# Kernel tuning notes

Measured on AMD Instinct MI355X. Metric: run time of the kernel, lower is better.

## Reference

```python
import jax, jax.numpy as jnp
import numpy as np


def setup_inputs() -> dict:
    key = jax.random.key(0)
    k1, k2, k3, k4 = jax.random.split(key, 4)
    d_in, d_out, B, T = 1024, 1024, 4, 2048
    scale = 1.0 / np.sqrt(d_in)
    return {
        "x": jax.random.normal(k1, (B, T, d_in), dtype=jnp.float32),
        "Wq": jax.random.normal(k2, (d_in, d_out), dtype=jnp.float32) * scale,
        "Wk": jax.random.normal(k3, (d_in, d_out), dtype=jnp.float32) * scale,
        "Wv": jax.random.normal(k4, (d_in, d_out), dtype=jnp.float32) * scale,
    }


def reference(x, Wq, Wk, Wv):
    # x: [B, T, d_in]; Wq/Wk/Wv: [d_in, d_out] (Linear, bias=False)
    q = jnp.einsum("btd,de->bte", x, Wq)
    k = jnp.einsum("btd,de->bte", x, Wk)
    v = jnp.einsum("btd,de->bte", x, Wv)
    d_out = k.shape[-1]
    scores = jnp.einsum("bqe,bke->bqk", q, k)  # [B, T, T]
    T = x.shape[1]
    causal = jnp.triu(jnp.ones((T, T), dtype=bool), k=1)  # True above diagonal
    scores = jnp.where(causal[None, :, :], -jnp.inf, scores)
    # original divides after masking; -inf stays -inf so math is identical
    att = jax.nn.softmax(scores / jnp.sqrt(jnp.asarray(d_out, scores.dtype)), axis=-1)
    # dropout p=0.0 -> identity
    return jnp.einsum("bqk,bke->bqe", att, v)
```

## Files before the change

kernel.cpp:

```cpp
#include <hip/hip_runtime.h>
#include <stdint.h>
#include <math.h>

typedef unsigned short u16;
typedef __bf16 bf16x8 __attribute__((ext_vector_type(8)));
typedef float f32x4 __attribute__((ext_vector_type(4)));

enum { M_QKV = 0, M_SCORE = 1, M_PV = 2 };

__device__ __forceinline__ u16 f2bf(float f) {
    union { float f; unsigned int u; } a; a.f = f;
    unsigned int u = a.u;
    u += 0x7FFFu + ((u >> 16) & 1u);
    return (u16)(u >> 16);
}

__device__ __forceinline__ void async_load16(const void* g, void* l) {
    __builtin_amdgcn_global_load_lds(
        (const __attribute__((address_space(1))) void*)g,
        (__attribute__((address_space(3))) void*)l,
        16, 0, 0);
}

template<int MODE, int TBM>
__device__ __forceinline__ void gemm_core(
    const u16* __restrict__ A, const u16* __restrict__ Bt,
    void* __restrict__ Cv, float* __restrict__ rowsum,
    int bm, int bn, int bz, int M, int N, int K, float kfac,
    u16* As, u16* Bs)
{
    constexpr int KB  = 64;
    constexpr int NI  = TBM / 32;
    constexpr int ACH = TBM / 32;
    constexpr int BCH = 4;

    const int tid  = threadIdx.x;
    const int lane = tid & 63;
    const int wv   = tid >> 6;
    const int wm   = wv >> 1;
    const int wn   = wv & 1;

    f32x4 acc[NI][4] = {};

    const int rowA0 = bm * TBM, rowB0 = bn * 128;
    const int lrow  = lane >> 3;
    const int lslot = lane & 7;
    const int sg    = (lslot ^ lrow) * 8;

    int kEnd = K;
    if (MODE == M_PV) { int ke = (bm + 1) * TBM; kEnd = ke < K ? ke : K; }

    const int lm   = lane & 15;
    const int quad = lane >> 4;
    const int rx   = lm & 7;

    for (int k0 = 0; k0 < kEnd; k0 += KB) {
        #pragma unroll
        for (int c = 0; c < ACH; ++c) {
            const int cc  = wv * ACH + c;
            const int row = cc * 8 + lrow;
            const u16* src;
            if (MODE == M_PV)
                src = &A[(size_t)(k0 >> 7) * 16384 + (size_t)row * 128 + (k0 & 127) + sg];
            else
                src = &A[(size_t)(rowA0 + row) * K + k0 + sg];
            async_load16(src, &As[cc * 512 + lane * 8]);
        }
        #pragma unroll
        for (int c = 0; c < BCH; ++c) {
            const int cc  = wv * BCH + c;
            const int row = cc * 8 + lrow;
            async_load16(&Bt[(size_t)(rowB0 + row) * K + k0 + sg], &Bs[cc * 512 + lane * 8]);
        }
        __syncthreads();

        #pragma unroll
        for (int h = 0; h < 2; ++h) {
            const int sl = (((h * 4 + quad) ^ rx) * 8);
            bf16x8 af[NI], bfr[4];
            #pragma unroll
            for (int i = 0; i < NI; ++i)
                af[i] = *reinterpret_cast<const bf16x8*>(
                    &As[(wm * (TBM / 2) + i * 16 + lm) * KB + sl]);
            #pragma unroll
            for (int j = 0; j < 4; ++j)
                bfr[j] = *reinterpret_cast<const bf16x8*>(
                    &Bs[(wn * 64 + j * 16 + lm) * KB + sl]);
            #pragma unroll
            for (int i = 0; i < NI; ++i)
                #pragma unroll
                for (int j = 0; j < 4; ++j)
                    acc[i][j] = __builtin_amdgcn_mfma_f32_16x16x32_bf16(af[i], bfr[j], acc[i][j], 0, 0, 0);
        }
        __syncthreads();
    }

    if (MODE == M_SCORE) {
        u16* E = (u16*)Cv;
        float rs[NI][4];
        #pragma unroll
        for (int i = 0; i < NI; ++i)
            #pragma unroll
            for (int g = 0; g < 4; ++g) rs[i][g] = 0.f;
        #pragma unroll
        for (int i = 0; i < NI; ++i)
            #pragma unroll
            for (int j = 0; j < 4; ++j) {
                const int rl = wm * (TBM / 2) + i * 16 + quad * 4;
                const int cl = wn * 64 + j * 16 + lm;
                const int c  = rowB0 + cl;
                #pragma unroll
                for (int g = 0; g < 4; ++g) {
                    const int r = rowA0 + rl + g;
                    float e = (c <= r) ? exp2f(acc[i][j][g] * kfac) : 0.f;
                    E[(size_t)(rl + g) * 128 + cl] = f2bf(e);
                    rs[i][g] += e;
                }
            }
        #pragma unroll
        for (int i = 0; i < NI; ++i)
            #pragma unroll
            for (int g = 0; g < 4; ++g) {
                float v = rs[i][g];
                v += __shfl_xor(v, 1); v += __shfl_xor(v, 2);
                v += __shfl_xor(v, 4); v += __shfl_xor(v, 8);
                rs[i][g] = v;
            }
        if (lm == 0) {
            #pragma unroll
            for (int i = 0; i < NI; ++i)
                #pragma unroll
                for (int g = 0; g < 4; ++g) {
                    const int r = rowA0 + wm * (TBM / 2) + i * 16 + quad * 4 + g;
                    atomicAdd(&rowsum[(size_t)bz * M + r], rs[i][g]);
                }
        }
    } else {
        float* C = (float*)Cv + (size_t)bz * ((size_t)M * N);
        #pragma unroll
        for (int i = 0; i < NI; ++i) {
            const int r0 = rowA0 + wm * (TBM / 2) + i * 16 + quad * 4;
            float inv[4];
            #pragma unroll
            for (int g = 0; g < 4; ++g)
                inv[g] = 1.f / rowsum[(size_t)bz * M + r0 + g];
            #pragma unroll
            for (int j = 0; j < 4; ++j) {
                const int c0 = rowB0 + wn * 64 + j * 16 + lm;
                #pragma unroll
                for (int g = 0; g < 4; ++g)
                    C[(size_t)(r0 + g) * N + c0] = acc[i][j][g] * inv[g];
            }
        }
    }
}

__global__ __launch_bounds__(512, 2)
void k_qkv2(const u16* __restrict__ Xb, const u16* __restrict__ Wt,
            u16* __restrict__ Q, int M, int N, int K)
{
    extern __shared__ __attribute__((aligned(16))) u16 S[];
    const int tid  = threadIdx.x;
    const int lane = tid & 63;
    const int wv   = tid >> 6;
    const int wm   = wv >> 2;
    const int wn   = wv & 3;
    const int bn   = blockIdx.x;
    const int bm   = blockIdx.y;
    const int rowA0 = bm * 128, rowB0 = bn * 256;

    const int lrow  = lane >> 3;
    const int lslot = lane & 7;
    const int sg    = (lslot ^ lrow) * 8;
    const int lm    = lane & 15;
    const int quad  = lane >> 4;
    const int rx    = lm & 7;

    f32x4 acc[4][4] = {};

    const int nt = K >> 6;

    auto stage = [&](int t, int b) {
        u16* As = S + b * 24576;
        u16* Bs = As + 8192;
        const int k0 = t << 6;
        #pragma unroll
        for (int c = 0; c < 2; ++c) {
            const int cc  = wv * 2 + c;
            const int row = cc * 8 + lrow;
            async_load16(&Xb[(size_t)(rowA0 + row) * K + k0 + sg], &As[cc * 512 + lane * 8]);
        }
        #pragma unroll
        for (int c = 0; c < 4; ++c) {
            const int cc  = wv * 4 + c;
            const int row = cc * 8 + lrow;
            async_load16(&Wt[(size_t)(rowB0 + row) * K + k0 + sg], &Bs[cc * 512 + lane * 8]);
        }
    };

    auto compute = [&](int b) {
        const u16* As = S + b * 24576;
        const u16* Bs = As + 8192;
        #pragma unroll
        for (int h = 0; h < 2; ++h) {
            const int sl = (((h * 4 + quad) ^ rx) * 8);
            bf16x8 af[4], bfr[4];
            #pragma unroll
            for (int i = 0; i < 4; ++i)
                af[i] = *reinterpret_cast<const bf16x8*>(
                    &As[(wm * 64 + i * 16 + lm) * 64 + sl]);
            #pragma unroll
            for (int j = 0; j < 4; ++j)
                bfr[j] = *reinterpret_cast<const bf16x8*>(
                    &Bs[(wn * 64 + j * 16 + lm) * 64 + sl]);
            #pragma unroll
            for (int i = 0; i < 4; ++i)
                #pragma unroll
                for (int j = 0; j < 4; ++j)
                    acc[i][j] = __builtin_amdgcn_mfma_f32_16x16x32_bf16(af[i], bfr[j], acc[i][j], 0, 0, 0);
        }
    };

    stage(0, 0);
    stage(1, 1);
    asm volatile("s_waitcnt vmcnt(6)" ::: "memory");
    __builtin_amdgcn_s_barrier();

    int cb = 0;
    #pragma unroll 1
    for (int t = 0; t < nt - 2; ++t) {
        int sb = cb + 2; if (sb >= 3) sb -= 3;
        stage(t + 2, sb);
        compute(cb);
        asm volatile("s_waitcnt vmcnt(6)" ::: "memory");
        __builtin_amdgcn_s_barrier();
        if (++cb == 3) cb = 0;
    }
    compute(cb);
    asm volatile("s_waitcnt vmcnt(0)" ::: "memory");
    __builtin_amdgcn_s_barrier();
    if (++cb == 3) cb = 0;
    compute(cb);

    u16* C = Q + (size_t)(bn >> 2) * ((size_t)M * 1024);
    const int cbase = (rowB0 & 1023) + wn * 64;
    #pragma unroll
    for (int i = 0; i < 4; ++i)
        #pragma unroll
        for (int j = 0; j < 4; ++j) {
            const int r0 = rowA0 + wm * 64 + i * 16 + quad * 4;
            const int c0 = cbase + j * 16 + lm;
            #pragma unroll
            for (int g = 0; g < 4; ++g)
                C[(size_t)(r0 + g) * 1024 + c0] = f2bf(acc[i][j][g]);
        }
}

__global__ __launch_bounds__(256)
void k_score_vt(const u16* __restrict__ Q, const u16* __restrict__ Kb,
                u16* __restrict__ Epk, float* __restrict__ rowsum,
                const u16* __restrict__ Vb, u16* __restrict__ Vt,
                int T, int D, float kfac, int nTri)
{
    __shared__ __attribute__((aligned(16))) u16 As[128 * 64];
    __shared__ __attribute__((aligned(16))) u16 Bs[128 * 64];
    __shared__ u16 tt[32][33];
    const int bz = blockIdx.z;

    if ((int)blockIdx.x < nTri) {
        const int idx = blockIdx.x;
        int bm = (int)((sqrtf(8.f * (float)idx + 1.f) - 1.f) * 0.5f);
        while (bm * (bm + 1) / 2 > idx) --bm;
        while ((bm + 1) * (bm + 2) / 2 <= idx) ++bm;
        const int bn = idx - bm * (bm + 1) / 2;
        u16* Etile = Epk + ((size_t)bz * nTri + idx) * 16384;
        gemm_core<M_SCORE, 128>(Q + (size_t)bz * T * D, Kb + (size_t)bz * T * D,
                                Etile, rowsum, bm, bn, bz, T, T, D, kfac, As, Bs);
    } else {
        const int t  = blockIdx.x - nTri;
        const int cx = t & 31;
        const int cy = t >> 5;
        const u16* V = Vb + (size_t)bz * T * D;
        u16*      Vo = Vt + (size_t)bz * D * T;
        const int c0 = cx * 32, r0 = cy * 32;
        const int tx = threadIdx.x & 31, ty = threadIdx.x >> 5;
        #pragma unroll
        for (int s = 0; s < 32; s += 8)
            tt[ty + s][tx] = V[(size_t)(r0 + ty + s) * D + c0 + tx];
        __syncthreads();
        #pragma unroll
        for (int s = 0; s < 32; s += 8)
            Vo[(size_t)(c0 + ty + s) * T + r0 + tx] = tt[tx][ty + s];
    }
}

__global__ __launch_bounds__(256)
void k_pv(const u16* __restrict__ Epk, const u16* __restrict__ Vt,
          float* __restrict__ out, const float* __restrict__ rowsum,
          int T, int D, int nTri)
{
    __shared__ __attribute__((aligned(16))) u16 As[128 * 64];
    __shared__ __attribute__((aligned(16))) u16 Bs[128 * 64];
    const int bz = blockIdx.z;
    const int bm = (gridDim.y - 1) - blockIdx.y;
    const u16* Arow = Epk + ((size_t)bz * nTri + (size_t)bm * (bm + 1) / 2) * 16384;
    gemm_core<M_PV, 128>(Arow, Vt + (size_t)bz * D * T,
                         out, (float*)rowsum, bm, blockIdx.x, bz,
                         T, D, T, 0.f, As, Bs);
}

__global__ __launch_bounds__(256)
void k_prep(const float* __restrict__ x,
            const float* __restrict__ W0, const float* __restrict__ W1,
            const float* __restrict__ W2,
            u16* __restrict__ Xb, u16* __restrict__ Wt, float* __restrict__ RS,
            int D, int nCX, int nW)
{
    const int bx = blockIdx.x;
    if (bx < nCX) {
        long long i = ((long long)bx * 256 + threadIdx.x) * 8;
        const float4 a = *(const float4*)(x + i);
        const float4 b = *(const float4*)(x + i + 4);
        union { u16 u[8]; float4 v; } r;
        r.u[0] = f2bf(a.x); r.u[1] = f2bf(a.y); r.u[2] = f2bf(a.z); r.u[3] = f2bf(a.w);
        r.u[4] = f2bf(b.x); r.u[5] = f2bf(b.y); r.u[6] = f2bf(b.z); r.u[7] = f2bf(b.w);
        *(float4*)(Xb + i) = r.v;
    } else if (bx < nCX + nW) {
        __shared__ u16 t[32][33];
        const int w  = bx - nCX;
        const int z  = w >> 10;
        const int rm = w & 1023;
        const float* W = z == 0 ? W0 : (z == 1 ? W1 : W2);
        u16* dst = Wt + (size_t)z * D * D;
        const int c0 = (rm & 31) * 32, r0 = (rm >> 5) * 32;
        const int tx = threadIdx.x & 31, ty = threadIdx.x >> 5;
        #pragma unroll
        for (int s = 0; s < 32; s += 8)
            t[ty + s][tx] = f2bf(W[(size_t)(r0 + ty + s) * D + c0 + tx]);
        __syncthreads();
        #pragma unroll
        for (int s = 0; s < 32; s += 8)
            dst[(size_t)(c0 + ty + s) * D + r0 + tx] = t[tx][ty + s];
    } else {
        const int t = bx - nCX - nW;
        ((float4*)RS)[t * 256 + threadIdx.x] = float4{0.f, 0.f, 0.f, 0.f};
    }
}

extern "C" void kernel_launch(void* const* d_in, const int* in_sizes, int n_in,
                              void* d_out, int out_size, void* d_ws, size_t ws_size,
                              hipStream_t stream)
{
    const int B = 4, T = 2048, D = 1024;
    const float* x  = (const float*)d_in[0];
    const float* Wq = (const float*)d_in[1];
    const float* Wk = (const float*)d_in[2];
    const float* Wv = (const float*)d_in[3];
    float* out = (float*)d_out;

    const size_t nX = (size_t)B * T * D;
    u16* Xb  = (u16*)d_ws;
    u16* Wt  = Xb + nX;
    u16* Epk = (u16*)d_ws;
    u16* Q   = Wt + 3 * (size_t)D * D;
    u16* Kb  = Q + nX;
    u16* Vb  = Kb + nX;
    u16* Vt  = Vb + nX;
    float* RS = (float*)(Vt + nX);

    const float kfac = 1.4426950408889634f / 32.0f;
    const int nTri128 = 136;
    const int nCX = (int)(nX / (8 * 256));
    const int nW  = 3 * (D / 32) * (D / 32);
    const int nRS = (B * T) / (4 * 256);

    static bool attr_done = false;
    if (!attr_done) {
        (void)hipFuncSetAttribute((const void*)k_qkv2,
                                  hipFuncAttributeMaxDynamicSharedMemorySize,
                                  147456);
        attr_done = true;
    }

    k_prep<<<dim3(nCX + nW + nRS), 256, 0, stream>>>(
        x, Wq, Wk, Wv, Xb, Wt, RS, D, nCX, nW);
    k_qkv2<<<dim3(3 * D / 256, (B * T) / 128), 512, 147456, stream>>>(
        Xb, Wt, Q, B * T, 3 * D, D);
    k_score_vt<<<dim3(nTri128 + (D / 32) * (T / 32), 1, B), 256, 0, stream>>>(
        Q, Kb, Epk, RS, Vb, Vt, T, D, kfac, nTri128);
    k_pv<<<dim3(D / 128, T / 128, B), 256, 0, stream>>>(
        Epk, Vt, out, RS, T, D, nTri128);
}
```

Measured before the change: 245.5 us.

## Double-buffer LDS tiles in score and PV GEMMs to overlap loads with MFMA

Replaces the single-buffered gemm_core with gemm2, which uses two LDS stages: it issues the async global-to-LDS loads for the next K tile before running the MFMAs on the current one, then waits on vmcnt and a barrier. This targets the load latency that sat exposed between the two __syncthreads per iteration. It doubles LDS use per block to 64 KB, which may reduce how many blocks fit on a CU, and it hardcodes the 128-row tile size.

```diff
diff --git a/kernel.cpp b/kernel.cpp
--- a/kernel.cpp
+++ b/kernel.cpp
@@ -6,7 +6,7 @@
 typedef __bf16 bf16x8 __attribute__((ext_vector_type(8)));
 typedef float f32x4 __attribute__((ext_vector_type(4)));
 
-enum { M_QKV = 0, M_SCORE = 1, M_PV = 2 };
+enum { M_SCORE = 1, M_PV = 2 };
 
 __device__ __forceinline__ u16 f2bf(float f) {
     union { float f; unsigned int u; } a; a.f = f;
@@ -22,91 +22,103 @@
         16, 0, 0);
 }
 
-template<int MODE, int TBM>
-__device__ __forceinline__ void gemm_core(
+template<int MODE>
+__device__ __forceinline__ void gemm2(
     const u16* __restrict__ A, const u16* __restrict__ Bt,
     void* __restrict__ Cv, float* __restrict__ rowsum,
     int bm, int bn, int bz, int M, int N, int K, float kfac,
     u16* As, u16* Bs)
 {
-    constexpr int KB  = 64;
-    constexpr int NI  = TBM / 32;
-    constexpr int ACH = TBM / 32;
-    constexpr int BCH = 4;
-
+    constexpr int KB = 64;
     const int tid  = threadIdx.x;
     const int lane = tid & 63;
     const int wv   = tid >> 6;
     const int wm   = wv >> 1;
     const int wn   = wv & 1;
 
-    f32x4 acc[NI][4] = {};
-
-    const int rowA0 = bm * TBM, rowB0 = bn * 128;
+    f32x4 acc[4][4] = {};
+
+    const int rowA0 = bm * 128, rowB0 = bn * 128;
     const int lrow  = lane >> 3;
     const int lslot = lane & 7;
     const int sg    = (lslot ^ lrow) * 8;
 
     int kEnd = K;
-    if (MODE == M_PV) { int ke = (bm + 1) * TBM; kEnd = ke < K ? ke : K; }
+    if (MODE == M_PV) { int ke = (bm + 1) * 128; kEnd = ke < K ? ke : K; }
+    const int nt = kEnd >> 6;
 
     const int lm   = lane & 15;
     const int quad = lane >> 4;
     const int rx   = lm & 7;
 
-    for (int k0 = 0; k0 < kEnd; k0 += KB) {
-        #pragma unroll
-        for (int c = 0; c < ACH; ++c) {
-            const int cc  = wv * ACH + c;
+    auto stage = [&](int t, int b) {
+        const int k0 = t << 6;
+        u16* as = As + b * 8192;
+        u16* bs = Bs + b * 8192;
+        #pragma unroll
+        for (int c = 0; c < 4; ++c) {
+            const int cc  = wv * 4 + c;
             const int row = cc * 8 + lrow;
-            const u16* src;
+            const u16* srcA;
             if (MODE == M_PV)
-                src = &A[(size_t)(k0 >> 7) * 16384 + (size_t)row * 128 + (k0 & 127) + sg];
+                srcA = &A[(size_t)(k0 >> 7) * 16384 + (size_t)row * 128 + (k0 & 127) + sg];
             else
-                src = &A[(size_t)(rowA0 + row) * K + k0 + sg];
-            async_load16(src, &As[cc * 512 + lane * 8]);
-        }
-        #pragma unroll
-        for (int c = 0; c < BCH; ++c) {
-            const int cc  = wv * BCH + c;
-            const int row = cc * 8 + lrow;
-            async_load16(&Bt[(size_t)(rowB0 + row) * K + k0 + sg], &Bs[cc * 512 + lane * 8]);
-        }
-        __syncthreads();
-
+                srcA = &A[(size_t)(rowA0 + row) * K + k0 + sg];
+            async_load16(srcA, &as[cc * 512 + lane * 8]);
+            async_load16(&Bt[(size_t)(rowB0 + row) * K + k0 + sg], &bs[cc * 512 + lane * 8]);
+        }
+    };
+
+    auto compute = [&](int b) {
+        const u16* as = As + b * 8192;
+        const u16* bs = Bs + b * 8192;
         #pragma unroll
         for (int h = 0; h < 2; ++h) {
             const int sl = (((h * 4 + quad) ^ rx) * 8);
-            bf16x8 af[NI], bfr[4];
-            #pragma unroll
-            for (int i = 0; i < NI; ++i)
+            bf16x8 af[4], bfr[4];
+            #pragma unroll
+            for (int i = 0; i < 4; ++i)
                 af[i] = *reinterpret_cast<const bf16x8*>(
-                    &As[(wm * (TBM / 2) + i * 16 + lm) * KB + sl]);
+                    &as[(wm * 64 + i * 16 + lm) * KB + sl]);
             #pragma unroll
             for (int j = 0; j < 4; ++j)
                 bfr[j] = *reinterpret_cast<const bf16x8*>(
-                    &Bs[(wn * 64 + j * 16 + lm) * KB + sl]);
-            #pragma unroll
-            for (int i = 0; i < NI; ++i)
+                    &bs[(wn * 64 + j * 16 + lm) * KB + sl]);
+            #pragma unroll
+            for (int i = 0; i < 4; ++i)
                 #pragma unroll
                 for (int j = 0; j < 4; ++j)
                     acc[i][j] = __builtin_amdgcn_mfma_f32_16x16x32_bf16(af[i], bfr[j], acc[i][j], 0, 0, 0);
         }
-        __syncthreads();
-    }
+    };
+
+    stage(0, 0);
+    asm volatile("s_waitcnt vmcnt(0)" ::: "memory");
+    __builtin_amdgcn_s_barrier();
+
+    int cb = 0;
+    #pragma unroll 1
+    for (int t = 0; t < nt - 1; ++t) {
+        stage(t + 1, cb ^ 1);
+        compute(cb);
+        asm volatile("s_waitcnt vmcnt(0)" ::: "memory");
+        __builtin_amdgcn_s_barrier();
+        cb ^= 1;
+    }
+    compute(cb);
 
     if (MODE == M_SCORE) {
         u16* E = (u16*)Cv;
-        float rs[NI][4];
-        #pragma unroll
-        for (int i = 0; i < NI; ++i)
+        float rs[4][4];
+        #pragma unroll
+        for (int i = 0; i < 4; ++i)
             #pragma unroll
             for (int g = 0; g < 4; ++g) rs[i][g] = 0.f;
         #pragma unroll
-        for (int i = 0; i < NI; ++i)
+        for (int i = 0; i < 4; ++i)
             #pragma unroll
             for (int j = 0; j < 4; ++j) {
-                const int rl = wm * (TBM / 2) + i * 16 + quad * 4;
+                const int rl = wm * 64 + i * 16 + quad * 4;
                 const int cl = wn * 64 + j * 16 + lm;
                 const int c  = rowB0 + cl;
                 #pragma unroll
@@ -118,7 +130,7 @@
                 }
             }
         #pragma unroll
-        for (int i = 0; i < NI; ++i)
+        for (int i = 0; i < 4; ++i)
             #pragma unroll
             for (int g = 0; g < 4; ++g) {
                 float v = rs[i][g];
@@ -128,18 +140,18 @@
             }
         if (lm == 0) {
             #pragma unroll
-            for (int i = 0; i < NI; ++i)
+            for (int i = 0; i < 4; ++i)
                 #pragma unroll
                 for (int g = 0; g < 4; ++g) {
-                    const int r = rowA0 + wm * (TBM / 2) + i * 16 + quad * 4 + g;
+                    const int r = rowA0 + wm * 64 + i * 16 + quad * 4 + g;
                     atomicAdd(&rowsum[(size_t)bz * M + r], rs[i][g]);
                 }
         }
     } else {
         float* C = (float*)Cv + (size_t)bz * ((size_t)M * N);
         #pragma unroll
-        for (int i = 0; i < NI; ++i) {
-            const int r0 = rowA0 + wm * (TBM / 2) + i * 16 + quad * 4;
+        for (int i = 0; i < 4; ++i) {
+            const int r0 = rowA0 + wm * 64 + i * 16 + quad * 4;
             float inv[4];
             #pragma unroll
             for (int g = 0; g < 4; ++g)
@@ -262,8 +274,8 @@
                 const u16* __restrict__ Vb, u16* __restrict__ Vt,
                 int T, int D, float kfac, int nTri)
 {
-    __shared__ __attribute__((aligned(16))) u16 As[128 * 64];
-    __shared__ __attribute__((aligned(16))) u16 Bs[128 * 64];
+    __shared__ __attribute__((aligned(16))) u16 As[2 * 128 * 64];
+    __shared__ __attribute__((aligned(16))) u16 Bs[2 * 128 * 64];
     __shared__ u16 tt[32][33];
     const int bz = blockIdx.z;
 
@@ -274,8 +286,8 @@
         while ((bm + 1) * (bm + 2) / 2 <= idx) ++bm;
         const int bn = idx - bm * (bm + 1) / 2;
         u16* Etile = Epk + ((size_t)bz * nTri + idx) * 16384;
-        gemm_core<M_SCORE, 128>(Q + (size_t)bz * T * D, Kb + (size_t)bz * T * D,
-                                Etile, rowsum, bm, bn, bz, T, T, D, kfac, As, Bs);
+        gemm2<M_SCORE>(Q + (size_t)bz * T * D, Kb + (size_t)bz * T * D,
+                       Etile, rowsum, bm, bn, bz, T, T, D, kfac, As, Bs);
     } else {
         const int t  = blockIdx.x - nTri;
         const int cx = t & 31;
@@ -299,14 +311,14 @@
           float* __restrict__ out, const float* __restrict__ rowsum,
           int T, int D, int nTri)
 {
-    __shared__ __attribute__((aligned(16))) u16 As[128 * 64];
-    __shared__ __attribute__((aligned(16))) u16 Bs[128 * 64];
+    __shared__ __attribute__((aligned(16))) u16 As[2 * 128 * 64];
+    __shared__ __attribute__((aligned(16))) u16 Bs[2 * 128 * 64];
     const int bz = blockIdx.z;
     const int bm = (gridDim.y - 1) - blockIdx.y;
     const u16* Arow = Epk + ((size_t)bz * nTri + (size_t)bm * (bm + 1) / 2) * 16384;
-    gemm_core<M_PV, 128>(Arow, Vt + (size_t)bz * D * T,
-                         out, (float*)rowsum, bm, blockIdx.x, bz,
-                         T, D, T, 0.f, As, Bs);
+    gemm2<M_PV>(Arow, Vt + (size_t)bz * D * T,
+                out, (float*)rowsum, bm, blockIdx.x, bz,
+                T, D, T, 0.f, As, Bs);
 }
 
 __global__ __launch_bounds__(256)
```

New measurement: 251.3 us. +2.4%, slower.

## Use 64-row M tiles for score and PV kernels to raise block count

Applied to the files above, without the earlier changes.

Shrinks the M tile of the score and PV GEMMs from 128 to 64 rows while keeping the packed 128x128 exp-score tile storage, so each 64-row half-tile writes into its half of the stored block. The score grid doubles to 272 triangular blocks using a new index-to-(bm,bn) mapping, and the PV grid doubles along T. The aim is more blocks for better load balance and occupancy on the causal triangle, and a finer causal cutoff in PV. The cost is halved B-operand reuse per block and more redundant K/V tile loads.

```diff
diff --git a/kernel.cpp b/kernel.cpp
--- a/kernel.cpp
+++ b/kernel.cpp
@@ -6,7 +6,7 @@
 typedef __bf16 bf16x8 __attribute__((ext_vector_type(8)));
 typedef float f32x4 __attribute__((ext_vector_type(4)));
 
-enum { M_QKV = 0, M_SCORE = 1, M_PV = 2 };
+enum { M_SCORE = 1, M_PV = 2 };
 
 __device__ __forceinline__ u16 f2bf(float f) {
     union { float f; unsigned int u; } a; a.f = f;
@@ -61,7 +61,8 @@
             const int row = cc * 8 + lrow;
             const u16* src;
             if (MODE == M_PV)
-                src = &A[(size_t)(k0 >> 7) * 16384 + (size_t)row * 128 + (k0 & 127) + sg];
+                src = &A[(size_t)(k0 >> 7) * 16384
+                         + (size_t)((rowA0 & 127) + row) * 128 + (k0 & 127) + sg];
             else
                 src = &A[(size_t)(rowA0 + row) * K + k0 + sg];
             async_load16(src, &As[cc * 512 + lane * 8]);
@@ -97,6 +98,7 @@
 
     if (MODE == M_SCORE) {
         u16* E = (u16*)Cv;
+        const int rbase = rowA0 & 127;
         float rs[NI][4];
         #pragma unroll
         for (int i = 0; i < NI; ++i)
@@ -113,7 +115,7 @@
                 for (int g = 0; g < 4; ++g) {
                     const int r = rowA0 + rl + g;
                     float e = (c <= r) ? exp2f(acc[i][j][g] * kfac) : 0.f;
-                    E[(size_t)(rl + g) * 128 + cl] = f2bf(e);
+                    E[(size_t)(rbase + rl + g) * 128 + cl] = f2bf(e);
                     rs[i][g] += e;
                 }
             }
@@ -262,20 +264,24 @@
                 const u16* __restrict__ Vb, u16* __restrict__ Vt,
                 int T, int D, float kfac, int nTri)
 {
-    __shared__ __attribute__((aligned(16))) u16 As[128 * 64];
+    __shared__ __attribute__((aligned(16))) u16 As[64 * 64];
     __shared__ __attribute__((aligned(16))) u16 Bs[128 * 64];
     __shared__ u16 tt[32][33];
     const int bz = blockIdx.z;
 
     if ((int)blockIdx.x < nTri) {
         const int idx = blockIdx.x;
-        int bm = (int)((sqrtf(8.f * (float)idx + 1.f) - 1.f) * 0.5f);
-        while (bm * (bm + 1) / 2 > idx) --bm;
-        while ((bm + 1) * (bm + 2) / 2 <= idx) ++bm;
-        const int bn = idx - bm * (bm + 1) / 2;
-        u16* Etile = Epk + ((size_t)bz * nTri + idx) * 16384;
-        gemm_core<M_SCORE, 128>(Q + (size_t)bz * T * D, Kb + (size_t)bz * T * D,
-                                Etile, rowsum, bm, bn, bz, T, T, D, kfac, As, Bs);
+        int w = (int)sqrtf((float)idx + 0.5f);
+        while (w * w > idx) --w;
+        while ((w + 1) * (w + 1) <= idx) ++w;
+        int bm, bn;
+        if (idx < w * w + w) { bm = 2 * w - 1; bn = idx - w * w; }
+        else                 { bm = 2 * w;     bn = idx - (w * w + w); }
+        const int bm128 = bm >> 1;
+        const int tile  = bm128 * (bm128 + 1) / 2 + bn;
+        u16* Etile = Epk + ((size_t)bz * 136 + tile) * 16384;
+        gemm_core<M_SCORE, 64>(Q + (size_t)bz * T * D, Kb + (size_t)bz * T * D,
+                               Etile, rowsum, bm, bn, bz, T, T, D, kfac, As, Bs);
     } else {
         const int t  = blockIdx.x - nTri;
         const int cx = t & 31;
@@ -297,16 +303,17 @@
 __global__ __launch_bounds__(256)
 void k_pv(const u16* __restrict__ Epk, const u16* __restrict__ Vt,
           float* __restrict__ out, const float* __restrict__ rowsum,
-          int T, int D, int nTri)
-{
-    __shared__ __attribute__((aligned(16))) u16 As[128 * 64];
+          int T, int D)
+{
+    __shared__ __attribute__((aligned(16))) u16 As[64 * 64];
     __shared__ __attribute__((aligned(16))) u16 Bs[128 * 64];
     const int bz = blockIdx.z;
     const int bm = (gridDim.y - 1) - blockIdx.y;
-    const u16* Arow = Epk + ((size_t)bz * nTri + (size_t)bm * (bm + 1) / 2) * 16384;
-    gemm_core<M_PV, 128>(Arow, Vt + (size_t)bz * D * T,
-                         out, (float*)rowsum, bm, blockIdx.x, bz,
-                         T, D, T, 0.f, As, Bs);
+    const int bm128 = bm >> 1;
+    const u16* Arow = Epk + ((size_t)bz * 136 + (size_t)bm128 * (bm128 + 1) / 2) * 16384;
+    gemm_core<M_PV, 64>(Arow, Vt + (size_t)bz * D * T,
+                        out, (float*)rowsum, bm, blockIdx.x, bz,
+                        T, D, T, 0.f, As, Bs);
 }
 
 __global__ __launch_bounds__(256)
@@ -369,7 +376,7 @@
     float* RS = (float*)(Vt + nX);
 
     const float kfac = 1.4426950408889634f / 32.0f;
-    const int nTri128 = 136;
+    const int nTri64 = 272;
     const int nCX = (int)(nX / (8 * 256));
     const int nW  = 3 * (D / 32) * (D / 32);
     const int nRS = (B * T) / (4 * 256);
@@ -386,8 +393,8 @@
         x, Wq, Wk, Wv, Xb, Wt, RS, D, nCX, nW);
     k_qkv2<<<dim3(3 * D / 256, (B * T) / 128), 512, 147456, stream>>>(
         Xb, Wt, Q, B * T, 3 * D, D);
-    k_score_vt<<<dim3(nTri128 + (D / 32) * (T / 32), 1, B), 256, 0, stream>>>(
-        Q, Kb, Epk, RS, Vb, Vt, T, D, kfac, nTri128);
-    k_pv<<<dim3(D / 128, T / 128, B), 256, 0, stream>>>(
-        Epk, Vt, out, RS, T, D, nTri128);
-}
+    k_score_vt<<<dim3(nTri64 + (D / 32) * (T / 32), 1, B), 256, 0, stream>>>(
+        Q, Kb, Epk, RS, Vb, Vt, T, D, kfac, nTri64);
+    k_pv<<<dim3(D / 128, T / 64, B), 256, 0, stream>>>(
+        Epk, Vt, out, RS, T, D);
+}
```

Result: faster. 233.5 us (-4.9%).
